# Kernel tuning notes

Measured on AMD Instinct MI355X. Metric: run time of the kernel, lower is better.

Reference implementation:

```python
import jax, jax.numpy as jnp
import numpy as np

L = 6        # num_coupling_layers
T_DIM = 64   # t_dim
HALF = T_DIM // 2
COND = 128   # cond_dim
HID = 1024   # hidden_dim
B = 32768


def setup_inputs() -> dict:
    key = jax.random.key(0)
    ks = jax.random.split(key, 8)
    s_in = 1.0 / np.sqrt(HALF + COND)
    s_h = 1.0 / np.sqrt(HID)
    T = jax.random.normal(ks[0], (B, T_DIM), dtype=jnp.float32)
    cond = jax.random.normal(ks[1], (B, COND), dtype=jnp.float32)
    W1 = jax.random.normal(ks[2], (L, HALF + COND, HID), dtype=jnp.float32) * s_in
    b1 = jnp.zeros((L, HID), dtype=jnp.float32)
    W2 = jax.random.normal(ks[3], (L, HID, HID), dtype=jnp.float32) * s_h
    b2 = jnp.zeros((L, HID), dtype=jnp.float32)
    W3 = jax.random.normal(ks[4], (L, HID, 2 * HALF), dtype=jnp.float32) * s_h
    b3 = jnp.zeros((L, 2 * HALF), dtype=jnp.float32)
    return {"T": T, "cond": cond, "W1": W1, "b1": b1, "W2": W2, "b2": b2, "W3": W3, "b3": b3}


def reference(T, cond, W1, b1, W2, b2, W3, b3):
    # Conditional normalizing flow: 6 affine coupling layers with alternating
    # contiguous half masks. Even layers transform the first half, odd the second.
    def mlp(h, i):
        x = jax.nn.relu(h @ W1[i] + b1[i])
        x = jax.nn.relu(x @ W2[i] + b2[i])
        return x @ W3[i] + b3[i]

    z = T
    log_det = jnp.zeros(T.shape[0], dtype=T.dtype)
    for i in range(L):
        if i % 2 == 0:
            masked, unmasked = z[:, :HALF], z[:, HALF:]
        else:
            masked, unmasked = z[:, HALF:], z[:, :HALF]
        params = mlp(jnp.concatenate([unmasked, cond], axis=1), i)
        s = jnp.tanh(params[:, :HALF])
        t_shift = params[:, HALF:]
        y_masked = masked * jnp.exp(s) + t_shift
        if i % 2 == 0:
            z = jnp.concatenate([y_masked, unmasked], axis=1)
        else:
            z = jnp.concatenate([unmasked, y_masked], axis=1)
        log_det = log_det + jnp.sum(s, axis=1)
    return z, log_det
```

## Files before the change

kernel.cpp:

```cpp
#include <hip/hip_runtime.h>
#include <hip/hip_fp16.h>
#include <stdint.h>

typedef _Float16 f16;
typedef _Float16 f16x8 __attribute__((ext_vector_type(8)));
typedef float f32x4 __attribute__((ext_vector_type(4)));

#define NB 32768
#define LAYERS 6
#define AK 160
#define HID 1024

__device__ __forceinline__ void async_copy16(const void* g, void* l) {
  __builtin_amdgcn_global_load_lds(
      (const __attribute__((address_space(1))) void*)g,
      (__attribute__((address_space(3))) void*)l, 16, 0, 0);
}

__global__ void prep_batch(const float* __restrict__ T, const float* __restrict__ cond,
                           float* __restrict__ z, float* __restrict__ ld,
                           f16* __restrict__ A)
{
  const int S1 = NB * 64;
  const int S2 = S1 + NB;
  const int S3 = S2 + NB * 32;
  const int S4 = S3 + NB * 128;
  for (int i = blockIdx.x * blockDim.x + threadIdx.x; i < S4;
       i += gridDim.x * blockDim.x) {
    if (i < S1) {
      z[i] = T[i];
    } else if (i < S2) {
      ld[i - S1] = 0.0f;
    } else if (i < S3) {
      int r = i - S2;
      int row = r >> 5, j = r & 31;
      A[(size_t)row * AK + j] = (f16)T[row * 64 + 32 + j];
    } else {
      int r = i - S3;
      int row = r >> 7, j = r & 127;
      A[(size_t)row * AK + 32 + j] = (f16)cond[r];
    }
  }
}

__global__ void wtrans(const float* __restrict__ W, f16* __restrict__ Wt,
                       const int K_, const int N_)
{
  __shared__ float t[64][65];
  const long off = (long)blockIdx.z * K_ * N_;
  const float* Wl = W + off;
  f16* Wtl = Wt + off;
  const int k0 = blockIdx.y * 64, n0 = blockIdx.x * 64;
  const int tx = threadIdx.x & 63, ty4 = threadIdx.x >> 6;
#pragma unroll
  for (int r = ty4; r < 64; r += 4) {
    const int k = k0 + r;
    if (k < K_) t[r][tx] = Wl[(long)k * N_ + n0 + tx];
  }
  __syncthreads();
  const int k = k0 + tx;
  if (k < K_) {
#pragma unroll
    for (int r = ty4; r < 64; r += 4) {
      const int n = n0 + r;
      Wtl[(long)n * K_ + k] = (f16)t[tx][r];
    }
  }
}

__global__ __launch_bounds__(256, 3)
void gemm12(const f16* __restrict__ A, const int K,
            const f16* __restrict__ Wt,
            const float* __restrict__ bias,
            f16* __restrict__ C)
{
  __shared__ __align__(16) f16 As[2][128 * 32];
  __shared__ __align__(16) f16 Bs[2][128 * 32];
  const int tid  = threadIdx.x;
  const int wave = tid >> 6;
  const int lane = tid & 63;
  const int c15  = lane & 15;
  const int quad = lane >> 4;
  const int wm = (wave & 1) * 64;
  const int wn = (wave >> 1) * 64;

  const int b = blockIdx.x;
  const int x = b & 7, i = b >> 3;
  const long rowStart = (long)(x * 32 + (i >> 3)) * 128;
  const long colStart = (long)(i & 7) * 128;

  const f16* Ab = A  + rowStart * K;
  const f16* Bb = Wt + colStart * K;

  const int ra  = tid >> 2;
  const int kca = (((tid & 3) ^ ((ra >> 1) & 3))) * 8;

  f32x4 acc[4][4] = {};
  const int nK = K >> 5;

  auto stage = [&](int kt, int sel) {
    const long ko = (long)kt * 32;
    f16* as = &As[sel][0];
    f16* bs = &Bs[sel][0];
#pragma unroll
    for (int q = 0; q < 2; ++q)
      async_copy16(Ab + (long)(q * 64 + ra) * K + ko + kca,
                   as + (q * 256 + wave * 64) * 8);
#pragma unroll
    for (int q = 0; q < 2; ++q)
      async_copy16(Bb + (long)(q * 64 + ra) * K + ko + kca,
                   bs + (q * 256 + wave * 64) * 8);
  };

  stage(0, 0);
  for (int kt = 0; kt < nK; ++kt) {
    __syncthreads();
    if (kt + 1 < nK) stage(kt + 1, (kt + 1) & 1);
    const f16* as = &As[kt & 1][0];
    const f16* bs = &Bs[kt & 1][0];

    f16x8 a[4], bf[4];
#pragma unroll
    for (int mi = 0; mi < 4; ++mi) {
      const int R = wm + mi * 16 + c15;
      a[mi] = *(const f16x8*)&as[R * 32 + ((quad ^ ((R >> 1) & 3)) << 3)];
    }
#pragma unroll
    for (int ni = 0; ni < 4; ++ni) {
      const int R = wn + ni * 16 + c15;
      bf[ni] = *(const f16x8*)&bs[R * 32 + ((quad ^ ((R >> 1) & 3)) << 3)];
    }
#pragma unroll
    for (int mi = 0; mi < 4; ++mi)
#pragma unroll
      for (int ni = 0; ni < 4; ++ni)
        acc[mi][ni] = __builtin_amdgcn_mfma_f32_16x16x32_f16(
            a[mi], bf[ni], acc[mi][ni], 0, 0, 0);
  }

#pragma unroll
  for (int ni = 0; ni < 4; ++ni) {
    const long gn = colStart + wn + ni * 16 + c15;
    const float bv = bias[gn];
#pragma unroll
    for (int mi = 0; mi < 4; ++mi) {
#pragma unroll
      for (int r = 0; r < 4; ++r) {
        const long gm = rowStart + wm + mi * 16 + quad * 4 + r;
        float v = acc[mi][ni][r] + bv;
        v = fmaxf(v, 0.0f);
        C[gm * HID + gn] = (f16)v;
      }
    }
  }
}

__global__ __launch_bounds__(256, 4)
void gemm3_coupling(const f16* __restrict__ X2, const f16* __restrict__ W3t,
                    const float* __restrict__ b3, float* __restrict__ z,
                    float* __restrict__ log_det, f16* __restrict__ Anext,
                    const int maskoff)
{
  __shared__ __align__(16) f16 As[2][128 * 32];
  __shared__ __align__(16) f16 Bs[2][64 * 32];
  const int tid = threadIdx.x;
  const int wave = tid >> 6, lane = tid & 63;
  const int c15 = lane & 15, quad = lane >> 4;
  const int wm = wave * 32;
  const long rowStart = (long)blockIdx.x * 128;

  const f16* Ab = X2 + rowStart * HID;
  const int ra  = tid >> 2;
  const int kca = (((tid & 3) ^ ((ra >> 1) & 3))) * 8;

  f32x4 acc[2][4] = {};

  auto stage = [&](int kt, int sel) {
    const long ko = (long)kt * 32;
    f16* as = &As[sel][0];
    f16* bs = &Bs[sel][0];
#pragma unroll
    for (int q = 0; q < 2; ++q)
      async_copy16(Ab + (long)(q * 64 + ra) * HID + ko + kca,
                   as + (q * 256 + wave * 64) * 8);
    async_copy16(W3t + (long)ra * HID + ko + kca,
                 bs + (wave * 64) * 8);
  };

  stage(0, 0);
  for (int kt = 0; kt < 32; ++kt) {
    __syncthreads();
    if (kt + 1 < 32) stage(kt + 1, (kt + 1) & 1);
    const f16* as = &As[kt & 1][0];
    const f16* bs = &Bs[kt & 1][0];

    f16x8 a[2], bf[4];
#pragma unroll
    for (int mi = 0; mi < 2; ++mi) {
      const int R = wm + mi * 16 + c15;
      a[mi] = *(const f16x8*)&as[R * 32 + ((quad ^ ((R >> 1) & 3)) << 3)];
    }
#pragma unroll
    for (int ni = 0; ni < 4; ++ni) {
      const int R = ni * 16 + c15;
      bf[ni] = *(const f16x8*)&bs[R * 32 + ((quad ^ ((R >> 1) & 3)) << 3)];
    }
#pragma unroll
    for (int mi = 0; mi < 2; ++mi)
#pragma unroll
      for (int ni = 0; ni < 4; ++ni)
        acc[mi][ni] = __builtin_amdgcn_mfma_f32_16x16x32_f16(a[mi], bf[ni], acc[mi][ni], 0, 0, 0);
  }

#pragma unroll
  for (int mi = 0; mi < 2; ++mi) {
    float sp[4] = {0.0f, 0.0f, 0.0f, 0.0f};
#pragma unroll
    for (int ni = 0; ni < 2; ++ni) {
      const int j = ni * 16 + c15;
      const float bs = b3[j];
      const float bt = b3[32 + j];
#pragma unroll
      for (int r = 0; r < 4; ++r) {
        const long gm = rowStart + wm + mi * 16 + quad * 4 + r;
        const float sv = acc[mi][ni][r] + bs;
        const float e2 = __expf(2.0f * sv);
        const float s  = 1.0f - 2.0f / (e2 + 1.0f);
        const float tv = acc[mi][ni + 2][r] + bt;
        const float m  = z[gm * 64 + maskoff + j];
        const float y  = fmaf(m, __expf(s), tv);
        z[gm * 64 + maskoff + j] = y;
        Anext[gm * AK + j] = (f16)y;
        sp[r] += s;
      }
    }
#pragma unroll
    for (int r = 0; r < 4; ++r) {
      float v = sp[r];
      v += __shfl_xor(v, 1);
      v += __shfl_xor(v, 2);
      v += __shfl_xor(v, 4);
      v += __shfl_xor(v, 8);
      if (c15 == 0) {
        const long gm = rowStart + wm + mi * 16 + quad * 4 + r;
        log_det[gm] += v;
      }
    }
  }
}

extern "C" void kernel_launch(void* const* d_in, const int* in_sizes, int n_in,
                              void* d_out, int out_size, void* d_ws, size_t ws_size,
                              hipStream_t stream) {
  (void)in_sizes; (void)n_in; (void)out_size; (void)ws_size;
  const float* T    = (const float*)d_in[0];
  const float* cond = (const float*)d_in[1];
  const float* W1   = (const float*)d_in[2];
  const float* b1   = (const float*)d_in[3];
  const float* W2   = (const float*)d_in[4];
  const float* b2   = (const float*)d_in[5];
  const float* W3   = (const float*)d_in[6];
  const float* b3   = (const float*)d_in[7];

  float* z  = (float*)d_out;
  float* ld = z + (size_t)NB * 64;

  f16* A   = (f16*)d_ws;
  f16* X1  = A   + (size_t)NB * AK;
  f16* X2  = X1  + (size_t)NB * HID;
  f16* W1t = X2  + (size_t)NB * HID;
  f16* W2t = W1t + (size_t)6 * 1024 * 160;
  f16* W3t = W2t + ((size_t)6 << 20);

  prep_batch<<<2048, 256, 0, stream>>>(T, cond, z, ld, A);
  wtrans<<<dim3(16, 3, 6),  256, 0, stream>>>(W1, W1t, AK, 1024);
  wtrans<<<dim3(16, 16, 6), 256, 0, stream>>>(W2, W2t, HID, 1024);
  wtrans<<<dim3(1, 16, 6),  256, 0, stream>>>(W3, W3t, HID, 64);

  const int g12 = (NB / 128) * (HID / 128);
  for (int l = 0; l < LAYERS; ++l) {
    gemm12<<<g12, 256, 0, stream>>>(A, AK, W1t + (size_t)l * 1024 * AK,
                                    b1 + l * 1024, X1);
    gemm12<<<g12, 256, 0, stream>>>(X1, HID, W2t + ((size_t)l << 20),
                                    b2 + l * 1024, X2);
    const int maskoff = (l & 1) ? 32 : 0;
    gemm3_coupling<<<NB / 128, 256, 0, stream>>>(X2, W3t + (size_t)l * 64 * 1024,
                                                 b3 + l * 64, z, ld, A, maskoff);
  }
}
```

Measured before the change: 899.7 us.

## Load full K=160 tiles for first GEMM and halve rows per block in GEMM3

Adds a dedicated first-layer GEMM that loads the entire K=160 slice of A and W into LDS in one shot, with no double-buffered loop, then runs five MFMA k-steps. This removes per-k-step barriers and pipeline overhead for the short K dimension. The coupling GEMM3 now uses 64-row blocks, giving twice as many blocks (512 versus 256) to better fill the CUs on a small-N GEMM. The trade-off is a larger LDS footprint (80KB per block in gemm1_full) and more redundant W3 loads.

```diff
diff --git a/kernel.cpp b/kernel.cpp
--- a/kernel.cpp
+++ b/kernel.cpp
@@ -68,6 +68,80 @@
   }
 }
 
+__global__ __launch_bounds__(256, 2)
+void gemm1_full(const f16* __restrict__ A,
+                const f16* __restrict__ Wt,
+                const float* __restrict__ bias,
+                f16* __restrict__ C)
+{
+  __shared__ __align__(16) f16 As[128 * 160];
+  __shared__ __align__(16) f16 Bs[128 * 160];
+  const int tid  = threadIdx.x;
+  const int lane = tid & 63;
+  const int wave = tid >> 6;
+  const int c15  = lane & 15;
+  const int quad = lane >> 4;
+  const int wm = (wave & 1) * 64;
+  const int wn = (wave >> 1) * 64;
+
+  const int b = blockIdx.x;
+  const int x = b & 7, i = b >> 3;
+  const long rowStart = (long)(x * 32 + (i >> 3)) * 128;
+  const long colStart = (long)(i & 7) * 128;
+
+  const f16* Ab = A  + rowStart * AK;
+  const f16* Bb = Wt + colStart * AK;
+
+#pragma unroll
+  for (int it = 0; it < 10; ++it) {
+    const int f = it * 256 + tid;
+    const int row = f / 20;
+    const int ch  = f - row * 20;
+    const int chs = ch ^ ((row >> 1) & 3);
+    async_copy16(Ab + (long)row * AK + chs * 8, &As[0] + (long)f * 8);
+    async_copy16(Bb + (long)row * AK + chs * 8, &Bs[0] + (long)f * 8);
+  }
+  __syncthreads();
+
+  f32x4 acc[4][4] = {};
+#pragma unroll
+  for (int kt = 0; kt < 5; ++kt) {
+    f16x8 a[4], bf[4];
+#pragma unroll
+    for (int mi = 0; mi < 4; ++mi) {
+      const int R = wm + mi * 16 + c15;
+      a[mi] = *(const f16x8*)&As[(R * 20 + kt * 4 + (quad ^ ((R >> 1) & 3))) * 8];
+    }
+#pragma unroll
+    for (int ni = 0; ni < 4; ++ni) {
+      const int R = wn + ni * 16 + c15;
+      bf[ni] = *(const f16x8*)&Bs[(R * 20 + kt * 4 + (quad ^ ((R >> 1) & 3))) * 8];
+    }
+#pragma unroll
+    for (int mi = 0; mi < 4; ++mi)
+#pragma unroll
+      for (int ni = 0; ni < 4; ++ni)
+        acc[mi][ni] = __builtin_amdgcn_mfma_f32_16x16x32_f16(
+            a[mi], bf[ni], acc[mi][ni], 0, 0, 0);
+  }
+
+#pragma unroll
+  for (int ni = 0; ni < 4; ++ni) {
+    const long gn = colStart + wn + ni * 16 + c15;
+    const float bv = bias[gn];
+#pragma unroll
+    for (int mi = 0; mi < 4; ++mi) {
+#pragma unroll
+      for (int r = 0; r < 4; ++r) {
+        const long gm = rowStart + wm + mi * 16 + quad * 4 + r;
+        float v = acc[mi][ni][r] + bv;
+        v = fmaxf(v, 0.0f);
+        C[gm * HID + gn] = (f16)v;
+      }
+    }
+  }
+}
+
 __global__ __launch_bounds__(256, 3)
 void gemm12(const f16* __restrict__ A, const int K,
             const f16* __restrict__ Wt,
@@ -161,30 +235,26 @@
                     float* __restrict__ log_det, f16* __restrict__ Anext,
                     const int maskoff)
 {
-  __shared__ __align__(16) f16 As[2][128 * 32];
+  __shared__ __align__(16) f16 As[2][64 * 32];
   __shared__ __align__(16) f16 Bs[2][64 * 32];
   const int tid = threadIdx.x;
   const int wave = tid >> 6, lane = tid & 63;
   const int c15 = lane & 15, quad = lane >> 4;
-  const int wm = wave * 32;
-  const long rowStart = (long)blockIdx.x * 128;
+  const int wm = wave * 16;
+  const long rowStart = (long)blockIdx.x * 64;
 
   const f16* Ab = X2 + rowStart * HID;
   const int ra  = tid >> 2;
   const int kca = (((tid & 3) ^ ((ra >> 1) & 3))) * 8;
 
-  f32x4 acc[2][4] = {};
+  f32x4 acc[4] = {};
 
   auto stage = [&](int kt, int sel) {
     const long ko = (long)kt * 32;
-    f16* as = &As[sel][0];
-    f16* bs = &Bs[sel][0];
-#pragma unroll
-    for (int q = 0; q < 2; ++q)
-      async_copy16(Ab + (long)(q * 64 + ra) * HID + ko + kca,
-                   as + (q * 256 + wave * 64) * 8);
+    async_copy16(Ab + (long)ra * HID + ko + kca,
+                 &As[sel][0] + (wave * 64) * 8);
     async_copy16(W3t + (long)ra * HID + ko + kca,
-                 bs + (wave * 64) * 8);
+                 &Bs[sel][0] + (wave * 64) * 8);
   };
 
   stage(0, 0);
@@ -194,57 +264,49 @@
     const f16* as = &As[kt & 1][0];
     const f16* bs = &Bs[kt & 1][0];
 
-    f16x8 a[2], bf[4];
-#pragma unroll
-    for (int mi = 0; mi < 2; ++mi) {
-      const int R = wm + mi * 16 + c15;
-      a[mi] = *(const f16x8*)&as[R * 32 + ((quad ^ ((R >> 1) & 3)) << 3)];
-    }
+    const int Ra = wm + c15;
+    f16x8 a = *(const f16x8*)&as[Ra * 32 + ((quad ^ ((Ra >> 1) & 3)) << 3)];
+    f16x8 bf[4];
 #pragma unroll
     for (int ni = 0; ni < 4; ++ni) {
       const int R = ni * 16 + c15;
       bf[ni] = *(const f16x8*)&bs[R * 32 + ((quad ^ ((R >> 1) & 3)) << 3)];
     }
 #pragma unroll
-    for (int mi = 0; mi < 2; ++mi)
-#pragma unroll
-      for (int ni = 0; ni < 4; ++ni)
-        acc[mi][ni] = __builtin_amdgcn_mfma_f32_16x16x32_f16(a[mi], bf[ni], acc[mi][ni], 0, 0, 0);
-  }
-
-#pragma unroll
-  for (int mi = 0; mi < 2; ++mi) {
-    float sp[4] = {0.0f, 0.0f, 0.0f, 0.0f};
-#pragma unroll
-    for (int ni = 0; ni < 2; ++ni) {
-      const int j = ni * 16 + c15;
-      const float bs = b3[j];
-      const float bt = b3[32 + j];
-#pragma unroll
-      for (int r = 0; r < 4; ++r) {
-        const long gm = rowStart + wm + mi * 16 + quad * 4 + r;
-        const float sv = acc[mi][ni][r] + bs;
-        const float e2 = __expf(2.0f * sv);
-        const float s  = 1.0f - 2.0f / (e2 + 1.0f);
-        const float tv = acc[mi][ni + 2][r] + bt;
-        const float m  = z[gm * 64 + maskoff + j];
-        const float y  = fmaf(m, __expf(s), tv);
-        z[gm * 64 + maskoff + j] = y;
-        Anext[gm * AK + j] = (f16)y;
-        sp[r] += s;
-      }
-    }
+    for (int ni = 0; ni < 4; ++ni)
+      acc[ni] = __builtin_amdgcn_mfma_f32_16x16x32_f16(a, bf[ni], acc[ni], 0, 0, 0);
+  }
+
+  float sp[4] = {0.0f, 0.0f, 0.0f, 0.0f};
+#pragma unroll
+  for (int ni = 0; ni < 2; ++ni) {
+    const int j = ni * 16 + c15;
+    const float bs = b3[j];
+    const float bt = b3[32 + j];
 #pragma unroll
     for (int r = 0; r < 4; ++r) {
-      float v = sp[r];
-      v += __shfl_xor(v, 1);
-      v += __shfl_xor(v, 2);
-      v += __shfl_xor(v, 4);
-      v += __shfl_xor(v, 8);
-      if (c15 == 0) {
-        const long gm = rowStart + wm + mi * 16 + quad * 4 + r;
-        log_det[gm] += v;
-      }
+      const long gm = rowStart + wm + quad * 4 + r;
+      const float sv = acc[ni][r] + bs;
+      const float e2 = __expf(2.0f * sv);
+      const float s  = 1.0f - 2.0f / (e2 + 1.0f);
+      const float tv = acc[ni + 2][r] + bt;
+      const float m  = z[gm * 64 + maskoff + j];
+      const float y  = fmaf(m, __expf(s), tv);
+      z[gm * 64 + maskoff + j] = y;
+      Anext[gm * AK + j] = (f16)y;
+      sp[r] += s;
+    }
+  }
+#pragma unroll
+  for (int r = 0; r < 4; ++r) {
+    float v = sp[r];
+    v += __shfl_xor(v, 1);
+    v += __shfl_xor(v, 2);
+    v += __shfl_xor(v, 4);
+    v += __shfl_xor(v, 8);
+    if (c15 == 0) {
+      const long gm = rowStart + wm + quad * 4 + r;
+      log_det[gm] += v;
     }
   }
 }
@@ -279,12 +341,12 @@
 
   const int g12 = (NB / 128) * (HID / 128);
   for (int l = 0; l < LAYERS; ++l) {
-    gemm12<<<g12, 256, 0, stream>>>(A, AK, W1t + (size_t)l * 1024 * AK,
-                                    b1 + l * 1024, X1);
+    gemm1_full<<<g12, 256, 0, stream>>>(A, W1t + (size_t)l * 1024 * AK,
+                                        b1 + l * 1024, X1);
     gemm12<<<g12, 256, 0, stream>>>(X1, HID, W2t + ((size_t)l << 20),
                                     b2 + l * 1024, X2);
     const int maskoff = (l & 1) ? 32 : 0;
-    gemm3_coupling<<<NB / 128, 256, 0, stream>>>(X2, W3t + (size_t)l * 64 * 1024,
-                                                 b3 + l * 64, z, ld, A, maskoff);
-  }
-}
+    gemm3_coupling<<<NB / 64, 256, 0, stream>>>(X2, W3t + (size_t)l * 64 * 1024,
+                                                b3 + l * 64, z, ld, A, maskoff);
+  }
+}
```

Result: faster. 870.4 us (-3.3%).

## Fuse all stages into one persistent cooperative kernel with grid syncs

Applied to the files above, without the earlier changes.

Replaces the 22 separate launches (prep, three weight transposes, and three GEMMs per layer) with a single persistent cooperative kernel. Blocks loop over tiles and separate stages with grid.sync(). The final-layer GEMM tile is shrunk to 64 rows so 512 tiles spread across more blocks. This removes launch gaps and the idle tail between kernels, but adds grid-wide barrier cost. It also makes every stage share one kernel's register and occupancy budget, which may lower GEMM efficiency.

```diff
diff --git a/kernel.cpp b/kernel.cpp
--- a/kernel.cpp
+++ b/kernel.cpp
@@ -1,6 +1,9 @@
 #include <hip/hip_runtime.h>
 #include <hip/hip_fp16.h>
+#include <hip/hip_cooperative_groups.h>
 #include <stdint.h>
+
+namespace cg = cooperative_groups;
 
 typedef _Float16 f16;
 typedef _Float16 f16x8 __attribute__((ext_vector_type(8)));
@@ -17,40 +20,16 @@
       (__attribute__((address_space(3))) void*)l, 16, 0, 0);
 }
 
-__global__ void prep_batch(const float* __restrict__ T, const float* __restrict__ cond,
-                           float* __restrict__ z, float* __restrict__ ld,
-                           f16* __restrict__ A)
+__device__ __forceinline__ void wtrans_tile(const float* __restrict__ W,
+                                            f16* __restrict__ Wt,
+                                            const int K_, const int N_,
+                                            const int bx, const int by,
+                                            const int bz, float (*t)[65])
 {
-  const int S1 = NB * 64;
-  const int S2 = S1 + NB;
-  const int S3 = S2 + NB * 32;
-  const int S4 = S3 + NB * 128;
-  for (int i = blockIdx.x * blockDim.x + threadIdx.x; i < S4;
-       i += gridDim.x * blockDim.x) {
-    if (i < S1) {
-      z[i] = T[i];
-    } else if (i < S2) {
-      ld[i - S1] = 0.0f;
-    } else if (i < S3) {
-      int r = i - S2;
-      int row = r >> 5, j = r & 31;
-      A[(size_t)row * AK + j] = (f16)T[row * 64 + 32 + j];
-    } else {
-      int r = i - S3;
-      int row = r >> 7, j = r & 127;
-      A[(size_t)row * AK + 32 + j] = (f16)cond[r];
-    }
-  }
-}
-
-__global__ void wtrans(const float* __restrict__ W, f16* __restrict__ Wt,
-                       const int K_, const int N_)
-{
-  __shared__ float t[64][65];
-  const long off = (long)blockIdx.z * K_ * N_;
+  const long off = (long)bz * K_ * N_;
   const float* Wl = W + off;
   f16* Wtl = Wt + off;
-  const int k0 = blockIdx.y * 64, n0 = blockIdx.x * 64;
+  const int k0 = by * 64, n0 = bx * 64;
   const int tx = threadIdx.x & 63, ty4 = threadIdx.x >> 6;
 #pragma unroll
   for (int r = ty4; r < 64; r += 4) {
@@ -68,14 +47,14 @@
   }
 }
 
-__global__ __launch_bounds__(256, 3)
-void gemm12(const f16* __restrict__ A, const int K,
-            const f16* __restrict__ Wt,
-            const float* __restrict__ bias,
-            f16* __restrict__ C)
+__device__ void gemm_tile(const f16* __restrict__ A, const int K,
+                          const f16* __restrict__ Wt,
+                          const float* __restrict__ bias,
+                          f16* __restrict__ C, const int t,
+                          f16* __restrict__ sm)
 {
-  __shared__ __align__(16) f16 As[2][128 * 32];
-  __shared__ __align__(16) f16 Bs[2][128 * 32];
+  f16* AsB[2] = {sm, sm + 4096};
+  f16* BsB[2] = {sm + 8192, sm + 12288};
   const int tid  = threadIdx.x;
   const int wave = tid >> 6;
   const int lane = tid & 63;
@@ -84,8 +63,7 @@
   const int wm = (wave & 1) * 64;
   const int wn = (wave >> 1) * 64;
 
-  const int b = blockIdx.x;
-  const int x = b & 7, i = b >> 3;
+  const int x = t & 7, i = t >> 3;
   const long rowStart = (long)(x * 32 + (i >> 3)) * 128;
   const long colStart = (long)(i & 7) * 128;
 
@@ -100,8 +78,8 @@
 
   auto stage = [&](int kt, int sel) {
     const long ko = (long)kt * 32;
-    f16* as = &As[sel][0];
-    f16* bs = &Bs[sel][0];
+    f16* as = AsB[sel];
+    f16* bs = BsB[sel];
 #pragma unroll
     for (int q = 0; q < 2; ++q)
       async_copy16(Ab + (long)(q * 64 + ra) * K + ko + kca,
@@ -112,12 +90,13 @@
                    bs + (q * 256 + wave * 64) * 8);
   };
 
+  __syncthreads();
   stage(0, 0);
   for (int kt = 0; kt < nK; ++kt) {
     __syncthreads();
     if (kt + 1 < nK) stage(kt + 1, (kt + 1) & 1);
-    const f16* as = &As[kt & 1][0];
-    const f16* bs = &Bs[kt & 1][0];
+    const f16* as = AsB[kt & 1];
+    const f16* bs = BsB[kt & 1];
 
     f16x8 a[4], bf[4];
 #pragma unroll
@@ -155,97 +134,152 @@
   }
 }
 
-__global__ __launch_bounds__(256, 4)
-void gemm3_coupling(const f16* __restrict__ X2, const f16* __restrict__ W3t,
-                    const float* __restrict__ b3, float* __restrict__ z,
-                    float* __restrict__ log_det, f16* __restrict__ Anext,
-                    const int maskoff)
+__device__ void gemm3_tile(const f16* __restrict__ X2, const f16* __restrict__ W3t,
+                           const float* __restrict__ b3, float* __restrict__ z,
+                           float* __restrict__ log_det, f16* __restrict__ Anext,
+                           const int maskoff, const int t, f16* __restrict__ sm)
 {
-  __shared__ __align__(16) f16 As[2][128 * 32];
-  __shared__ __align__(16) f16 Bs[2][64 * 32];
+  f16* AsB[2] = {sm, sm + 2048};
+  f16* BsB[2] = {sm + 4096, sm + 6144};
   const int tid = threadIdx.x;
   const int wave = tid >> 6, lane = tid & 63;
   const int c15 = lane & 15, quad = lane >> 4;
-  const int wm = wave * 32;
-  const long rowStart = (long)blockIdx.x * 128;
+  const int wm = wave * 16;
+  const long rowStart = (long)t * 64;
 
   const f16* Ab = X2 + rowStart * HID;
   const int ra  = tid >> 2;
   const int kca = (((tid & 3) ^ ((ra >> 1) & 3))) * 8;
 
-  f32x4 acc[2][4] = {};
+  f32x4 acc[4] = {};
 
   auto stage = [&](int kt, int sel) {
     const long ko = (long)kt * 32;
-    f16* as = &As[sel][0];
-    f16* bs = &Bs[sel][0];
-#pragma unroll
-    for (int q = 0; q < 2; ++q)
-      async_copy16(Ab + (long)(q * 64 + ra) * HID + ko + kca,
-                   as + (q * 256 + wave * 64) * 8);
+    async_copy16(Ab + (long)ra * HID + ko + kca,
+                 AsB[sel] + (wave * 64) * 8);
     async_copy16(W3t + (long)ra * HID + ko + kca,
-                 bs + (wave * 64) * 8);
+                 BsB[sel] + (wave * 64) * 8);
   };
 
+  __syncthreads();
   stage(0, 0);
   for (int kt = 0; kt < 32; ++kt) {
     __syncthreads();
     if (kt + 1 < 32) stage(kt + 1, (kt + 1) & 1);
-    const f16* as = &As[kt & 1][0];
-    const f16* bs = &Bs[kt & 1][0];
-
-    f16x8 a[2], bf[4];
-#pragma unroll
-    for (int mi = 0; mi < 2; ++mi) {
-      const int R = wm + mi * 16 + c15;
-      a[mi] = *(const f16x8*)&as[R * 32 + ((quad ^ ((R >> 1) & 3)) << 3)];
-    }
+    const f16* as = AsB[kt & 1];
+    const f16* bs = BsB[kt & 1];
+
+    const int Ra = wm + c15;
+    f16x8 a = *(const f16x8*)&as[Ra * 32 + ((quad ^ ((Ra >> 1) & 3)) << 3)];
+    f16x8 bf[4];
 #pragma unroll
     for (int ni = 0; ni < 4; ++ni) {
       const int R = ni * 16 + c15;
       bf[ni] = *(const f16x8*)&bs[R * 32 + ((quad ^ ((R >> 1) & 3)) << 3)];
     }
 #pragma unroll
-    for (int mi = 0; mi < 2; ++mi)
-#pragma unroll
-      for (int ni = 0; ni < 4; ++ni)
-        acc[mi][ni] = __builtin_amdgcn_mfma_f32_16x16x32_f16(a[mi], bf[ni], acc[mi][ni], 0, 0, 0);
-  }
-
-#pragma unroll
-  for (int mi = 0; mi < 2; ++mi) {
-    float sp[4] = {0.0f, 0.0f, 0.0f, 0.0f};
-#pragma unroll
-    for (int ni = 0; ni < 2; ++ni) {
-      const int j = ni * 16 + c15;
-      const float bs = b3[j];
-      const float bt = b3[32 + j];
-#pragma unroll
-      for (int r = 0; r < 4; ++r) {
-        const long gm = rowStart + wm + mi * 16 + quad * 4 + r;
-        const float sv = acc[mi][ni][r] + bs;
-        const float e2 = __expf(2.0f * sv);
-        const float s  = 1.0f - 2.0f / (e2 + 1.0f);
-        const float tv = acc[mi][ni + 2][r] + bt;
-        const float m  = z[gm * 64 + maskoff + j];
-        const float y  = fmaf(m, __expf(s), tv);
-        z[gm * 64 + maskoff + j] = y;
-        Anext[gm * AK + j] = (f16)y;
-        sp[r] += s;
+    for (int ni = 0; ni < 4; ++ni)
+      acc[ni] = __builtin_amdgcn_mfma_f32_16x16x32_f16(a, bf[ni], acc[ni], 0, 0, 0);
+  }
+
+  float sp[4] = {0.0f, 0.0f, 0.0f, 0.0f};
+#pragma unroll
+  for (int ni = 0; ni < 2; ++ni) {
+    const int j = ni * 16 + c15;
+    const float bs = b3[j];
+    const float bt = b3[32 + j];
+#pragma unroll
+    for (int r = 0; r < 4; ++r) {
+      const long gm = rowStart + wm + quad * 4 + r;
+      const float sv = acc[ni][r] + bs;
+      const float e2 = __expf(2.0f * sv);
+      const float s  = 1.0f - 2.0f / (e2 + 1.0f);
+      const float tv = acc[ni + 2][r] + bt;
+      const float m  = z[gm * 64 + maskoff + j];
+      const float y  = fmaf(m, __expf(s), tv);
+      z[gm * 64 + maskoff + j] = y;
+      Anext[gm * AK + j] = (f16)y;
+      sp[r] += s;
+    }
+  }
+#pragma unroll
+  for (int r = 0; r < 4; ++r) {
+    float v = sp[r];
+    v += __shfl_xor(v, 1);
+    v += __shfl_xor(v, 2);
+    v += __shfl_xor(v, 4);
+    v += __shfl_xor(v, 8);
+    if (c15 == 0) {
+      const long gm = rowStart + wm + quad * 4 + r;
+      log_det[gm] += v;
+    }
+  }
+}
+
+__global__ void __launch_bounds__(256, 4)
+flow_all(const float* __restrict__ T, const float* __restrict__ cond,
+         const float* __restrict__ W1, const float* __restrict__ W2,
+         const float* __restrict__ W3, const float* __restrict__ b1,
+         const float* __restrict__ b2, const float* __restrict__ b3,
+         float* __restrict__ z, float* __restrict__ ld,
+         f16* __restrict__ A, f16* __restrict__ X1, f16* __restrict__ X2,
+         f16* __restrict__ W1t, f16* __restrict__ W2t, f16* __restrict__ W3t)
+{
+  __shared__ __align__(16) unsigned char smemraw[32768];
+  f16* sm = (f16*)smemraw;
+  cg::grid_group grid = cg::this_grid();
+
+  {
+    const int S1 = NB * 64;
+    const int S2 = S1 + NB;
+    const int S3 = S2 + NB * 32;
+    const int S4 = S3 + NB * 128;
+    for (int i = blockIdx.x * blockDim.x + threadIdx.x; i < S4;
+         i += gridDim.x * blockDim.x) {
+      if (i < S1) {
+        z[i] = T[i];
+      } else if (i < S2) {
+        ld[i - S1] = 0.0f;
+      } else if (i < S3) {
+        int r = i - S2;
+        int row = r >> 5, j = r & 31;
+        A[(size_t)row * AK + j] = (f16)T[row * 64 + 32 + j];
+      } else {
+        int r = i - S3;
+        int row = r >> 7, j = r & 127;
+        A[(size_t)row * AK + 32 + j] = (f16)cond[r];
       }
     }
-#pragma unroll
-    for (int r = 0; r < 4; ++r) {
-      float v = sp[r];
-      v += __shfl_xor(v, 1);
-      v += __shfl_xor(v, 2);
-      v += __shfl_xor(v, 4);
-      v += __shfl_xor(v, 8);
-      if (c15 == 0) {
-        const long gm = rowStart + wm + mi * 16 + quad * 4 + r;
-        log_det[gm] += v;
+    for (int tt = blockIdx.x; tt < 1920; tt += gridDim.x) {
+      __syncthreads();
+      float (*tile)[65] = (float(*)[65])smemraw;
+      if (tt < 288) {
+        wtrans_tile(W1, W1t, AK, 1024, tt % 16, (tt / 16) % 3, tt / 48, tile);
+      } else if (tt < 1824) {
+        const int l = tt - 288;
+        wtrans_tile(W2, W2t, HID, 1024, l % 16, (l / 16) % 16, l / 256, tile);
+      } else {
+        const int l = tt - 1824;
+        wtrans_tile(W3, W3t, HID, 64, 0, l % 16, l / 16, tile);
       }
     }
+  }
+  grid.sync();
+
+  for (int l = 0; l < LAYERS; ++l) {
+    const f16* w1 = W1t + (size_t)l * 1024 * AK;
+    const f16* w2 = W2t + ((size_t)l << 20);
+    const f16* w3 = W3t + (size_t)l * 64 * 1024;
+    for (int t = blockIdx.x; t < 2048; t += gridDim.x)
+      gemm_tile(A, AK, w1, b1 + l * 1024, X1, t, sm);
+    grid.sync();
+    for (int t = blockIdx.x; t < 2048; t += gridDim.x)
+      gemm_tile(X1, HID, w2, b2 + l * 1024, X2, t, sm);
+    grid.sync();
+    const int maskoff = (l & 1) ? 32 : 0;
+    for (int t = blockIdx.x; t < 512; t += gridDim.x)
+      gemm3_tile(X2, w3, b3 + l * 64, z, ld, A, maskoff, t, sm);
+    grid.sync();
   }
 }
 
@@ -272,19 +306,16 @@
   f16* W2t = W1t + (size_t)6 * 1024 * 160;
   f16* W3t = W2t + ((size_t)6 << 20);
 
-  prep_batch<<<2048, 256, 0, stream>>>(T, cond, z, ld, A);
-  wtrans<<<dim3(16, 3, 6),  256, 0, stream>>>(W1, W1t, AK, 1024);
-  wtrans<<<dim3(16, 16, 6), 256, 0, stream>>>(W2, W2t, HID, 1024);
-  wtrans<<<dim3(1, 16, 6),  256, 0, stream>>>(W3, W3t, HID, 64);
-
-  const int g12 = (NB / 128) * (HID / 128);
-  for (int l = 0; l < LAYERS; ++l) {
-    gemm12<<<g12, 256, 0, stream>>>(A, AK, W1t + (size_t)l * 1024 * AK,
-                                    b1 + l * 1024, X1);
-    gemm12<<<g12, 256, 0, stream>>>(X1, HID, W2t + ((size_t)l << 20),
-                                    b2 + l * 1024, X2);
-    const int maskoff = (l & 1) ? 32 : 0;
-    gemm3_coupling<<<NB / 128, 256, 0, stream>>>(X2, W3t + (size_t)l * 64 * 1024,
-                                                 b3 + l * 64, z, ld, A, maskoff);
-  }
-}
+  int nb = 0;
+  hipOccupancyMaxActiveBlocksPerMultiprocessor(&nb, flow_all, 256, 0);
+  if (nb < 1) nb = 1;
+  if (nb > 4) nb = 4;
+  const int gblocks = 256 * nb;
+
+  void* args[] = {
+      (void*)&T, (void*)&cond, (void*)&W1, (void*)&W2, (void*)&W3,
+      (void*)&b1, (void*)&b2, (void*)&b3,
+      (void*)&z, (void*)&ld, (void*)&A, (void*)&X1, (void*)&X2,
+      (void*)&W1t, (void*)&W2t, (void*)&W3t};
+  hipLaunchCooperativeKernel(flow_all, dim3(gblocks), dim3(256), args, 0, stream);
+}
```

Result: slower. 2.316 ms (+157.4%).
